# Performance work log

Measured on AMD Instinct MI355X. Metric: run time of the kernel, lower is better.

The kernel has to match this reference:

```python
import jax, jax.numpy as jnp
import numpy as np

B = 16384      # batch (original code uses B=1; break generalized per-sample)
H = 1024       # MLP hidden width from MLP([2, 1024, 1])
NMAX = 10      # RModel nmax default


def _mlp(x, W1, b1, W2, b2):
    # Linear(2->H) + ELU, then Linear(H->1) (no final activation: act=None)
    h = jax.nn.elu(x @ W1.T + b1)
    return h @ W2.T + b2


def setup_inputs() -> dict:
    key = jax.random.key(0)
    ks = jax.random.split(key, 5)
    X = jax.random.normal(ks[0], (B, 1), dtype=jnp.float32)
    Y = jnp.zeros((B, 1), dtype=jnp.float32)
    # _init_layers: Linear weights ~ N(0, 0.5), biases = 0
    de_W1 = 0.5 * jax.random.normal(ks[1], (H, 2), dtype=jnp.float32)
    de_b1 = jnp.zeros((H,), dtype=jnp.float32)
    de_W2 = 0.5 * jax.random.normal(ks[2], (1, H), dtype=jnp.float32)
    de_b2 = jnp.zeros((1,), dtype=jnp.float32)
    val_W1 = 0.5 * jax.random.normal(ks[3], (H, 2), dtype=jnp.float32)
    val_b1 = jnp.zeros((H,), dtype=jnp.float32)
    val_W2 = 0.5 * jax.random.normal(ks[4], (1, H), dtype=jnp.float32)
    val_b2 = jnp.zeros((1,), dtype=jnp.float32)
    return {"X": X, "Y": Y,
            "de_W1": de_W1, "de_b1": de_b1, "de_W2": de_W2, "de_b2": de_b2,
            "val_W1": val_W1, "val_b1": val_b1, "val_W2": val_W2, "val_b2": val_b2}


def reference(X, Y, de_W1, de_b1, de_W2, de_b2, val_W1, val_b1, val_W2, val_b2):
    # xen/yen are identity (defaults)
    xsig = X
    v0 = _mlp(jnp.concatenate([xsig, Y], axis=1), val_W1, val_b1, val_W2, val_b2)
    done0 = jnp.zeros((X.shape[0], 1), dtype=bool)

    def step(carry, i):
        y_prev, v_prev, done = carry
        y_new = y_prev + _mlp(jnp.concatenate([xsig, y_prev], axis=1),
                              de_W1, de_b1, de_W2, de_b2)
        v_new = _mlp(jnp.concatenate([xsig, y_new], axis=1),
                     val_W1, val_b1, val_W2, val_b2)
        # samples that already broke keep (freeze) their last appended (Y, V)
        y = jnp.where(done, y_prev, y_new)
        v = jnp.where(done, v_prev, v_new)
        # break condition: i > 0 and V >= previous V (appended first, then break)
        done = done | ((i > 0) & (v_new >= v_prev))
        return (y, v, done), (y, v)

    _, (ys, vs) = jax.lax.scan(step, (Y, v0, done0), jnp.arange(NMAX))
    y_stack = jnp.concatenate([Y[None], ys], axis=0)   # [NMAX+1, B, 1]
    v_stack = jnp.concatenate([v0[None], vs], axis=0)  # [NMAX+1, B, 1]
    return (y_stack, v_stack)
```

## Files before the change

kernel.cpp:

```cpp
#include <hip/hip_runtime.h>

#define NMAX 10
#define KPL  16
#define L2E  1.4426950408889634f
#define LN2  0.6931471805599453f

typedef float f2 __attribute__((ext_vector_type(2)));

template<int CTRL, int RMASK, int BMASK>
__device__ __forceinline__ float dppmov(float v) {
    return __int_as_float(__builtin_amdgcn_update_dpp(
        0, __float_as_int(v), CTRL, RMASK, BMASK, true));
}
__device__ __forceinline__ float rdlane63(float v) {
    return __int_as_float(__builtin_amdgcn_readlane(__float_as_int(v), 63));
}

__device__ __forceinline__ void wred2(float& a, float& b) {
    a += dppmov<0xB1, 0xf, 0xf>(a);  b += dppmov<0xB1, 0xf, 0xf>(b);
    a += dppmov<0x4E, 0xf, 0xf>(a);  b += dppmov<0x4E, 0xf, 0xf>(b);
    a += dppmov<0x141,0xf, 0xf>(a);  b += dppmov<0x141,0xf, 0xf>(b);
    a += dppmov<0x140,0xf, 0xf>(a);  b += dppmov<0x140,0xf, 0xf>(b);
    a += dppmov<0x142,0xa, 0xf>(a);  b += dppmov<0x142,0xa, 0xf>(b);
    a += dppmov<0x143,0xc, 0xf>(a);  b += dppmov<0x143,0xc, 0xf>(b);
    a = rdlane63(a);                 b = rdlane63(b);
}

__device__ __forceinline__ void mlp_joint(
    const f2 (&wy)[KPL], const f2 (&u)[KPL], const f2 (&w2)[KPL],
    float y, float dbias, float vbias, float& dout, float& vout)
{
    const f2 yv = {y, y};
    float ad0 = 0.f, ad1 = 0.f, av0 = 0.f, av1 = 0.f;
#pragma unroll
    for (int k = 0; k < KPL; k += 2) {
        f2 p0 = wy[k]     * yv + u[k];
        f2 p1 = wy[k + 1] * yv + u[k + 1];
        float e0x = __builtin_amdgcn_exp2f(p0.x);
        float e0y = __builtin_amdgcn_exp2f(p0.y);
        float e1x = __builtin_amdgcn_exp2f(p1.x);
        float e1y = __builtin_amdgcn_exp2f(p1.y);
        float m0x = __builtin_amdgcn_fmed3f(p0.x, fmaf(e0x, L2E, -L2E), 0.f);
        float m0y = __builtin_amdgcn_fmed3f(p0.y, fmaf(e0y, L2E, -L2E), 0.f);
        float m1x = __builtin_amdgcn_fmed3f(p1.x, fmaf(e1x, L2E, -L2E), 0.f);
        float m1y = __builtin_amdgcn_fmed3f(p1.y, fmaf(e1y, L2E, -L2E), 0.f);
        ad0 = fmaf(w2[k].x,     m0x, ad0);
        av0 = fmaf(w2[k].y,     m0y, av0);
        ad1 = fmaf(w2[k + 1].x, m1x, ad1);
        av1 = fmaf(w2[k + 1].y, m1y, av1);
    }
    float a = ad0 + ad1, b = av0 + av1;
    wred2(a, b);
    dout = a + dbias; vout = b + vbias;
}

__global__ __launch_bounds__(256) void rmodel_kernel(
    const float* __restrict__ X, const float* __restrict__ Y,
    const float* __restrict__ de_W1, const float* __restrict__ de_b1,
    const float* __restrict__ de_W2, const float* __restrict__ de_b2,
    const float* __restrict__ val_W1, const float* __restrict__ val_b1,
    const float* __restrict__ val_W2, const float* __restrict__ val_b2,
    float* __restrict__ out, int n)
{
    const int wid  = threadIdx.x >> 6;
    const int lane = threadIdx.x & 63;
    const int b    = blockIdx.x * 4 + wid;
    if (b >= n) return;

    f2 wy[KPL], u[KPL], w2[KPL];

    const float x  = X[b];
    const float y0 = Y[b];

#pragma unroll
    for (int k = 0; k < KPL; ++k) {
        const int h = k * 64 + lane;
        float2 w1d = reinterpret_cast<const float2*>(de_W1)[h];
        float2 w1v = reinterpret_cast<const float2*>(val_W1)[h];
        wy[k] = (f2){w1d.y * L2E, w1v.y * L2E};
        u[k]  = (f2){fmaf(w1d.x, x, de_b1[h]) * L2E,
                     fmaf(w1v.x, x, val_b1[h]) * L2E};
        w2[k] = (f2){de_W2[h] * LN2, val_W2[h] * LN2};
    }
    const float db2 = de_b2[0];
    const float vb2 = val_b2[0];

    float* __restrict__ yout = out;
    float* __restrict__ vout = out + (size_t)(NMAX + 1) * n;

    float d, v;
    mlp_joint(wy, u, w2, y0, db2, vb2, d, v);
    if (lane == 0) { yout[b] = y0; vout[b] = v; }

    float y     = y0 + d;
    float vprev = v;
    float yfin  = y0, vfin = v;
    int   kend  = NMAX;

    float* yp = yout + b;
    float* vp = vout + b;
    for (int k = 1; k <= NMAX; ++k) {
        yp += n; vp += n;
        float dk, vk;
        mlp_joint(wy, u, w2, y, db2, vb2, dk, vk);
        if (lane == 0) { *yp = y; *vp = vk; }
        yfin = y; vfin = vk;
        if (k >= 2 && vk >= vprev) { kend = k; break; }
        vprev = vk;
        y += dk;
    }

    const int r = kend + 1 + lane;
    if (r <= NMAX) {
        yout[(size_t)r * n + b] = yfin;
        vout[(size_t)r * n + b] = vfin;
    }
}

extern "C" void kernel_launch(void* const* d_in, const int* in_sizes, int n_in,
                              void* d_out, int out_size, void* d_ws, size_t ws_size,
                              hipStream_t stream) {
    const float* X      = (const float*)d_in[0];
    const float* Y      = (const float*)d_in[1];
    const float* de_W1  = (const float*)d_in[2];
    const float* de_b1  = (const float*)d_in[3];
    const float* de_W2  = (const float*)d_in[4];
    const float* de_b2  = (const float*)d_in[5];
    const float* val_W1 = (const float*)d_in[6];
    const float* val_b1 = (const float*)d_in[7];
    const float* val_W2 = (const float*)d_in[8];
    const float* val_b2 = (const float*)d_in[9];
    float* out = (float*)d_out;

    const int n = in_sizes[0];
    dim3 block(256);
    dim3 grid((n + 3) / 4);
    hipLaunchKernelGGL(rmodel_kernel, grid, block, 0, stream,
                       X, Y, de_W1, de_b1, de_W2, de_b2,
                       val_W1, val_b1, val_W2, val_b2, out, n);
}
```

Before: 72.83 us.

## Use persistent grid-stride warps, packed f2 FMAs, and occupancy launch bounds

Launches a fixed grid of 1024 blocks that grid-stride over samples instead of one wavefront per sample. Rewrites the per-sample MLP inner loop with vector f2 FMAs so the compiler can emit packed FP32 instructions for the layer-1, ELU-offset and layer-2 accumulation steps. Adds a min-blocks hint of 4 to the launch bounds. The aim is to cut block launch overhead and VALU instruction count. In exchange, per-sample work with different early-exit lengths may be imbalanced across persistent warps, and the occupancy hint may cap registers.

```diff
diff --git a/kernel.cpp b/kernel.cpp
--- a/kernel.cpp
+++ b/kernel.cpp
@@ -4,6 +4,7 @@
 #define KPL  16
 #define L2E  1.4426950408889634f
 #define LN2  0.6931471805599453f
+#define NBLK 1024
 
 typedef float f2 __attribute__((ext_vector_type(2)));
 
@@ -30,31 +31,34 @@
     const f2 (&wy)[KPL], const f2 (&u)[KPL], const f2 (&w2)[KPL],
     float y, float dbias, float vbias, float& dout, float& vout)
 {
-    const f2 yv = {y, y};
-    float ad0 = 0.f, ad1 = 0.f, av0 = 0.f, av1 = 0.f;
+    const f2 yv   = {y, y};
+    const f2 l2e  = {L2E, L2E};
+    const f2 nl2e = {-L2E, -L2E};
+    f2 acc0 = {0.f, 0.f}, acc1 = {0.f, 0.f};
 #pragma unroll
     for (int k = 0; k < KPL; k += 2) {
-        f2 p0 = wy[k]     * yv + u[k];
-        f2 p1 = wy[k + 1] * yv + u[k + 1];
-        float e0x = __builtin_amdgcn_exp2f(p0.x);
-        float e0y = __builtin_amdgcn_exp2f(p0.y);
-        float e1x = __builtin_amdgcn_exp2f(p1.x);
-        float e1y = __builtin_amdgcn_exp2f(p1.y);
-        float m0x = __builtin_amdgcn_fmed3f(p0.x, fmaf(e0x, L2E, -L2E), 0.f);
-        float m0y = __builtin_amdgcn_fmed3f(p0.y, fmaf(e0y, L2E, -L2E), 0.f);
-        float m1x = __builtin_amdgcn_fmed3f(p1.x, fmaf(e1x, L2E, -L2E), 0.f);
-        float m1y = __builtin_amdgcn_fmed3f(p1.y, fmaf(e1y, L2E, -L2E), 0.f);
-        ad0 = fmaf(w2[k].x,     m0x, ad0);
-        av0 = fmaf(w2[k].y,     m0y, av0);
-        ad1 = fmaf(w2[k + 1].x, m1x, ad1);
-        av1 = fmaf(w2[k + 1].y, m1y, av1);
+        f2 p0 = __builtin_elementwise_fma(wy[k],     yv, u[k]);
+        f2 p1 = __builtin_elementwise_fma(wy[k + 1], yv, u[k + 1]);
+        f2 e0, e1;
+        e0.x = __builtin_amdgcn_exp2f(p0.x);  e0.y = __builtin_amdgcn_exp2f(p0.y);
+        e1.x = __builtin_amdgcn_exp2f(p1.x);  e1.y = __builtin_amdgcn_exp2f(p1.y);
+        f2 z0 = __builtin_elementwise_fma(e0, l2e, nl2e);
+        f2 z1 = __builtin_elementwise_fma(e1, l2e, nl2e);
+        f2 m0, m1;
+        m0.x = __builtin_amdgcn_fmed3f(p0.x, z0.x, 0.f);
+        m0.y = __builtin_amdgcn_fmed3f(p0.y, z0.y, 0.f);
+        m1.x = __builtin_amdgcn_fmed3f(p1.x, z1.x, 0.f);
+        m1.y = __builtin_amdgcn_fmed3f(p1.y, z1.y, 0.f);
+        acc0 = __builtin_elementwise_fma(w2[k],     m0, acc0);
+        acc1 = __builtin_elementwise_fma(w2[k + 1], m1, acc1);
     }
-    float a = ad0 + ad1, b = av0 + av1;
+    float a = acc0.x + acc1.x;
+    float b = acc0.y + acc1.y;
     wred2(a, b);
     dout = a + dbias; vout = b + vbias;
 }
 
-__global__ __launch_bounds__(256) void rmodel_kernel(
+__global__ __launch_bounds__(256, 4) void rmodel_kernel(
     const float* __restrict__ X, const float* __restrict__ Y,
     const float* __restrict__ de_W1, const float* __restrict__ de_b1,
     const float* __restrict__ de_W2, const float* __restrict__ de_b2,
@@ -64,56 +68,59 @@
 {
     const int wid  = threadIdx.x >> 6;
     const int lane = threadIdx.x & 63;
-    const int b    = blockIdx.x * 4 + wid;
-    if (b >= n) return;
+    const int gw   = blockIdx.x * 4 + wid;
+    const int GW   = NBLK * 4;
 
-    f2 wy[KPL], u[KPL], w2[KPL];
-
-    const float x  = X[b];
-    const float y0 = Y[b];
-
-#pragma unroll
-    for (int k = 0; k < KPL; ++k) {
-        const int h = k * 64 + lane;
-        float2 w1d = reinterpret_cast<const float2*>(de_W1)[h];
-        float2 w1v = reinterpret_cast<const float2*>(val_W1)[h];
-        wy[k] = (f2){w1d.y * L2E, w1v.y * L2E};
-        u[k]  = (f2){fmaf(w1d.x, x, de_b1[h]) * L2E,
-                     fmaf(w1v.x, x, val_b1[h]) * L2E};
-        w2[k] = (f2){de_W2[h] * LN2, val_W2[h] * LN2};
-    }
     const float db2 = de_b2[0];
     const float vb2 = val_b2[0];
 
     float* __restrict__ yout = out;
     float* __restrict__ vout = out + (size_t)(NMAX + 1) * n;
 
-    float d, v;
-    mlp_joint(wy, u, w2, y0, db2, vb2, d, v);
-    if (lane == 0) { yout[b] = y0; vout[b] = v; }
+    for (int b = gw; b < n; b += GW) {
+        f2 wy[KPL], u[KPL], w2[KPL];
 
-    float y     = y0 + d;
-    float vprev = v;
-    float yfin  = y0, vfin = v;
-    int   kend  = NMAX;
+        const float x  = X[b];
+        const float y0 = Y[b];
 
-    float* yp = yout + b;
-    float* vp = vout + b;
-    for (int k = 1; k <= NMAX; ++k) {
-        yp += n; vp += n;
-        float dk, vk;
-        mlp_joint(wy, u, w2, y, db2, vb2, dk, vk);
-        if (lane == 0) { *yp = y; *vp = vk; }
-        yfin = y; vfin = vk;
-        if (k >= 2 && vk >= vprev) { kend = k; break; }
-        vprev = vk;
-        y += dk;
-    }
+#pragma unroll
+        for (int k = 0; k < KPL; ++k) {
+            const int h = k * 64 + lane;
+            float2 w1d = reinterpret_cast<const float2*>(de_W1)[h];
+            float2 w1v = reinterpret_cast<const float2*>(val_W1)[h];
+            wy[k] = (f2){w1d.y * L2E, w1v.y * L2E};
+            u[k]  = (f2){fmaf(w1d.x, x, de_b1[h]) * L2E,
+                         fmaf(w1v.x, x, val_b1[h]) * L2E};
+            w2[k] = (f2){de_W2[h] * LN2, val_W2[h] * LN2};
+        }
 
-    const int r = kend + 1 + lane;
-    if (r <= NMAX) {
-        yout[(size_t)r * n + b] = yfin;
-        vout[(size_t)r * n + b] = vfin;
+        float d, v;
+        mlp_joint(wy, u, w2, y0, db2, vb2, d, v);
+        if (lane == 0) { yout[b] = y0; vout[b] = v; }
+
+        float y     = y0 + d;
+        float vprev = v;
+        float yfin  = y0, vfin = v;
+        int   kend  = NMAX;
+
+        float* yp = yout + b;
+        float* vp = vout + b;
+        for (int k = 1; k <= NMAX; ++k) {
+            yp += n; vp += n;
+            float dk, vk;
+            mlp_joint(wy, u, w2, y, db2, vb2, dk, vk);
+            if (lane == 0) { *yp = y; *vp = vk; }
+            yfin = y; vfin = vk;
+            if (k >= 2 && vk >= vprev) { kend = k; break; }
+            vprev = vk;
+            y += dk;
+        }
+
+        const int r = kend + 1 + lane;
+        if (r <= NMAX) {
+            yout[(size_t)r * n + b] = yfin;
+            vout[(size_t)r * n + b] = vfin;
+        }
     }
 }
 
@@ -134,7 +141,7 @@
 
     const int n = in_sizes[0];
     dim3 block(256);
-    dim3 grid((n + 3) / 4);
+    dim3 grid(NBLK);
     hipLaunchKernelGGL(rmodel_kernel, grid, block, 0, stream,
                        X, Y, de_W1, de_b1, de_W2, de_b2,
                        val_W1, val_b1, val_W2, val_b2, out, n);
```

Result: slower. 84.95 us (+16.6%).
